# Performance work log

Measured on AMD Instinct MI355X. Metric: run time of the kernel, lower is better.

## Reference

```python
import jax, jax.numpy as jnp
import numpy as np

NUM_POINTS = 100000
BATCH = 4096
K = 10


def setup_inputs() -> dict:
    key = jax.random.key(0)
    k1, k2, k3, k4, k5 = jax.random.split(key, 5)
    rays_o = jax.random.normal(k1, (BATCH, 3), dtype=jnp.float32)
    rays_d = jax.random.normal(k2, (BATCH, 3), dtype=jnp.float32)
    xyz = jax.random.normal(k3, (NUM_POINTS, 3), dtype=jnp.float32) * 0.1
    features_dc = jax.random.normal(k4, (NUM_POINTS, 1, 3), dtype=jnp.float32)
    opacity = jax.random.normal(k5, (NUM_POINTS, 1), dtype=jnp.float32)
    return {"rays_o": rays_o, "rays_d": rays_d, "xyz": xyz,
            "features_dc": features_dc, "opacity": opacity}


def reference(rays_o, rays_d, xyz, features_dc, opacity):
    # colors = sigmoid(features[:,0,:]) ; features[:,0,:] == features_dc[:,0,:]
    colors = jax.nn.sigmoid(features_dc[:, 0, :])          # [N,3]
    op = jax.nn.sigmoid(opacity[:, 0])                      # [N]
    ray_centers = rays_o + rays_d * 3.0                     # [B,3]
    # Euclidean cdist via ||a||^2 + ||b||^2 - 2 a.b (matmul form, like torch.cdist p=2)
    sq = (jnp.sum(ray_centers * ray_centers, axis=1)[:, None]
          + jnp.sum(xyz * xyz, axis=1)[None, :]
          - 2.0 * ray_centers @ xyz.T)                      # [B,N]
    distances = jnp.sqrt(jnp.maximum(sq, 0.0))
    # top-K smallest distances per ray
    _, idx = jax.lax.top_k(-distances, K)                   # [B,K]
    d_sel = jnp.take_along_axis(distances, idx, axis=1)     # [B,K]
    w = jnp.exp(-d_sel * 0.1) * op[idx]                     # [B,K]
    w = w / (jnp.sum(w, axis=1, keepdims=True) + 1e-8)
    rgb = jnp.einsum('bk,bkc->bc', w, colors[idx])          # [B,3]
    return rgb
```

## Files before the change

### kernel.cpp

```cpp
#include <hip/hip_runtime.h>
#include <math.h>

#define NPTS    100000
#define NRAYS   4096
#define KTOP    10
#define KMER    12
#define CAP     128

#define GCELLS  4096
#define RCAP    256
#define DMARGIN 1e-3f
#define NB      64
#define PPB     1568

#define TPAIR   4
#define NPART   64
#define TRAYS   8
#define TGRP    16

typedef float v2f __attribute__((ext_vector_type(2)));
typedef unsigned int u32;
typedef unsigned short u16;

static_assert(TGRP * 2048 <= NPTS, "theta sample within real points");
static_assert(NB * PPB >= NPTS, "binning covers all points");

__device__ __forceinline__ float4 make_center(const float* __restrict__ ro,
                                              const float* __restrict__ rd,
                                              int ray, float w) {
    float ox = ro[3 * ray + 0], oy = ro[3 * ray + 1], oz = ro[3 * ray + 2];
    float dx = rd[3 * ray + 0], dy = rd[3 * ray + 1], dz = rd[3 * ray + 2];
    float cx, cy, cz;
    {
#pragma clang fp contract(off)
        cx = ox + dx * 3.0f;
        cy = oy + dy * 3.0f;
        cz = oz + dz * 3.0f;
    }
    return make_float4(cx, cy, cz, w);
}

__device__ __forceinline__ float sigm(float x) { return 1.0f / (1.0f + expf(-x)); }

__device__ __forceinline__ float rfl(float x) {
    return __int_as_float(__builtin_amdgcn_readfirstlane(__float_as_int(x)));
}

__device__ __forceinline__ v2f score2(v2f px, v2f py, v2f pz, v2f pw,
                                      v2f rx, v2f ry, v2f rz) {
    v2f t = __builtin_elementwise_fma(pz, rz, pw);
    t = __builtin_elementwise_fma(py, ry, t);
    return __builtin_elementwise_fma(px, rx, t);
}

__device__ __forceinline__ unsigned long long mkkey(float sc, int id, bool v) {
    unsigned u = __float_as_uint(sc);
    u = (u & 0x80000000u) ? ~u : (u | 0x80000000u);
    unsigned long long k = ((unsigned long long)u << 32) | (unsigned)(~id);
    return v ? k : 0ull;
}

__device__ __forceinline__ int cellcoord(float x) {
    int v = (int)floorf((x + 0.8f) * 10.0f);
    return v < 0 ? 0 : (v > 15 ? 15 : v);
}

__global__ __launch_bounds__(256, 2) void theta_kernel(const float* __restrict__ xyz,
                                                       const float* __restrict__ ro,
                                                       const float* __restrict__ rd,
                                                       float4* __restrict__ c4,
                                                       int* __restrict__ cnt) {
    __shared__ float4 rsh[TRAYS];
    __shared__ float  Msh[4][TRAYS][64];
    const int tid = threadIdx.x, wave = tid >> 6, lane = tid & 63;
    const int rbase = blockIdx.x * TRAYS;

    if (tid < TRAYS) rsh[tid] = make_center(ro, rd, rbase + tid, 0.0f);
    __syncthreads();

    float4 rr[TRAYS];
#pragma unroll
    for (int r = 0; r < TRAYS; ++r) rr[r] = rsh[r];

    v2f M[TRAYS];
#pragma unroll
    for (int r = 0; r < TRAYS; ++r) M[r] = (v2f){-INFINITY, -INFINITY};

    v2f pxA[TPAIR], pyA[TPAIR], pzA[TPAIR], pwA[TPAIR];
    v2f pxB[TPAIR], pyB[TPAIR], pzB[TPAIR], pwB[TPAIR];

    auto loadg = [&](v2f* PX, v2f* PY, v2f* PZ, v2f* PW, int g) {
        const int id0 = g * 2048 + wave * 512 + lane;
#pragma unroll
        for (int u = 0; u < TPAIR; ++u) {
            int ia = id0 + (2 * u) * 64, ib = id0 + (2 * u + 1) * 64;
            float xa = xyz[3 * ia + 0], ya = xyz[3 * ia + 1], za = xyz[3 * ia + 2];
            float xb = xyz[3 * ib + 0], yb = xyz[3 * ib + 1], zb = xyz[3 * ib + 2];
            PX[u] = (v2f){xa, xb}; PY[u] = (v2f){ya, yb}; PZ[u] = (v2f){za, zb};
            PW[u] = (v2f){-0.5f * fmaf(xa, xa, fmaf(ya, ya, za * za)),
                          -0.5f * fmaf(xb, xb, fmaf(yb, yb, zb * zb))};
        }
    };
    auto computeg = [&](const v2f* PX, const v2f* PY, const v2f* PZ, const v2f* PW) {
#pragma unroll
        for (int r = 0; r < TRAYS; ++r) {
            const v2f rx = (v2f){rr[r].x, rr[r].x};
            const v2f ry = (v2f){rr[r].y, rr[r].y};
            const v2f rz = (v2f){rr[r].z, rr[r].z};
            v2f m = M[r];
#pragma unroll
            for (int u = 0; u < TPAIR; ++u)
                m = __builtin_elementwise_max(m, score2(PX[u], PY[u], PZ[u], PW[u], rx, ry, rz));
            M[r] = m;
        }
    };

    loadg(pxA, pyA, pzA, pwA, 0);
#pragma unroll 1
    for (int g = 0; g < TGRP; g += 2) {
        loadg(pxB, pyB, pzB, pwB, g + 1);
        computeg(pxA, pyA, pzA, pwA);
        if (g + 2 < TGRP) loadg(pxA, pyA, pzA, pwA, g + 2);
        computeg(pxB, pyB, pzB, pwB);
    }

#pragma unroll
    for (int r = 0; r < TRAYS; ++r)
        Msh[wave][r][lane] = fmaxf(M[r].x, M[r].y);
    __syncthreads();

    if (tid < TRAYS) {
        float vs[KTOP];
#pragma unroll
        for (int j = 0; j < KTOP; ++j) vs[j] = -INFINITY;
#pragma unroll 1
        for (int p = 0; p < NPART; ++p) {
            float v = fmaxf(fmaxf(Msh[0][tid][p], Msh[1][tid][p]),
                            fmaxf(Msh[2][tid][p], Msh[3][tid][p]));
#pragma unroll
            for (int t = KTOP - 1; t >= 1; --t) {
                bool up = v > vs[t - 1], here = v > vs[t];
                vs[t] = up ? vs[t - 1] : (here ? v : vs[t]);
            }
            vs[0] = fmaxf(vs[0], v);
        }
        float4 c = rsh[tid];
        c.w = vs[KTOP - 1];
        c4[rbase + tid] = c;
        cnt[rbase + tid] = 0;
    }
}

__global__ __launch_bounds__(256) void hist_kernel(const float* __restrict__ xyz,
                                                   u32* __restrict__ mat,
                                                   u16* __restrict__ cid16) {
    __shared__ u32 h[GCELLS];
    const int b = blockIdx.x, tid = threadIdx.x;
    for (int c = tid; c < GCELLS; c += 256) h[c] = 0;
    __syncthreads();
    const int s = b * PPB, e = (s + PPB < NPTS) ? s + PPB : NPTS;
    for (int i = s + tid; i < e; i += 256) {
        float x = xyz[3 * i + 0], y = xyz[3 * i + 1], z = xyz[3 * i + 2];
        int cid = (cellcoord(x) << 8) | (cellcoord(y) << 4) | cellcoord(z);
        cid16[i] = (u16)cid;
        atomicAdd(&h[cid], 1u);
    }
    __syncthreads();
    u32* row = mat + (size_t)b * GCELLS;
    for (int c = tid; c < GCELLS; c += 256) row[c] = h[c];
}

__global__ __launch_bounds__(256) void colsum_kernel(const u32* __restrict__ mat,
                                                     u32* __restrict__ cellcnt) {
    const int c = blockIdx.x * 256 + threadIdx.x;
    u32 s = 0;
#pragma unroll 4
    for (int b = 0; b < NB; ++b) s += mat[(size_t)b * GCELLS + c];
    cellcnt[c] = s;
}

__global__ __launch_bounds__(256) void prefix_kernel(const u32* __restrict__ cellcnt,
                                                     u32* __restrict__ cellstart) {
    __shared__ u32 wsum[4];
    const int tid = threadIdx.x, wave = tid >> 6, lane = tid & 63;
    const int base = tid * 16;
    u32 loc[16]; u32 s = 0;
#pragma unroll
    for (int k = 0; k < 16; ++k) { loc[k] = cellcnt[base + k]; s += loc[k]; }
    u32 v = s;
#pragma unroll
    for (int off = 1; off < 64; off <<= 1) {
        u32 o = __shfl_up(v, off);
        if (lane >= off) v += o;
    }
    if (lane == 63) wsum[wave] = v;
    __syncthreads();
    u32 woff = 0;
    for (int w = 0; w < 4; ++w) if (w < wave) woff += wsum[w];
    u32 run = woff + v - s;
#pragma unroll
    for (int k = 0; k < 16; ++k) {
        cellstart[base + k] = run;
        run += loc[k];
    }
    if (tid == 255) cellstart[4096] = run;
}

__global__ __launch_bounds__(256) void offs_kernel(u32* __restrict__ mat,
                                                   const u32* __restrict__ cellstart) {
    const int c = blockIdx.x * 256 + threadIdx.x;
    u32 run = cellstart[c];
#pragma unroll 4
    for (int b = 0; b < NB; ++b) {
        size_t idx = (size_t)b * GCELLS + c;
        u32 v = mat[idx];
        mat[idx] = run;
        run += v;
    }
}

__global__ __launch_bounds__(256) void scatter_kernel(const float* __restrict__ xyz,
                                                      const u16* __restrict__ cid16,
                                                      const u32* __restrict__ mat,
                                                      float4* __restrict__ pts4,
                                                      int* __restrict__ pid) {
    __shared__ u32 cur[GCELLS];
    const int b = blockIdx.x, tid = threadIdx.x;
    const u32* row = mat + (size_t)b * GCELLS;
    for (int c = tid; c < GCELLS; c += 256) cur[c] = row[c];
    __syncthreads();
    const int s = b * PPB, e = (s + PPB < NPTS) ? s + PPB : NPTS;
    for (int i = s + tid; i < e; i += 256) {
        int cid = cid16[i];
        u32 dst = atomicAdd(&cur[cid], 1u);
        float x = xyz[3 * i + 0], y = xyz[3 * i + 1], z = xyz[3 * i + 2];
        pts4[dst] = make_float4(x, y, z, -0.5f * fmaf(x, x, fmaf(y, y, z * z)));
        pid[dst] = i;
    }
}

__global__ __launch_bounds__(256) void scan_kernel(const float4* __restrict__ pts4,
                                                   const int* __restrict__ pid,
                                                   const u32* __restrict__ cellstart,
                                                   const float4* __restrict__ c4,
                                                   int* __restrict__ cnt,
                                                   float2* __restrict__ cand) {
    __shared__ u32    runS[4][RCAP], runE[4][RCAP];
    __shared__ float2 lbuf[4][CAP];
    __shared__ float  axd2[4][3][16];
    __shared__ int    nrun[4], lcnt[4];
    const int tid = threadIdx.x, w = tid >> 6, lane = tid & 63;
    const int ray = blockIdx.x * 4 + w;

    float4 q = c4[ray];
    const float cx = rfl(q.x), cy = rfl(q.y), cz = rfl(q.z), th = rfl(q.w);
    const float limit = fmaf(cx, cx, fmaf(cy, cy, cz * cz)) - 2.0f * th + DMARGIN;

    if (lane == 0) { nrun[w] = 0; lcnt[w] = 0; }
    if (lane < 48) {
        const int ax = lane >> 4, i = lane & 15;
        const float cc = (ax == 0) ? cx : ((ax == 1) ? cy : cz);
        const float lo = (i == 0)  ? -3.0e38f : -0.8f + 0.1f * (float)i;
        const float hi = (i == 15) ?  3.0e38f : -0.8f + 0.1f * (float)(i + 1);
        const float d = fmaxf(fmaxf(lo - cc, cc - hi), 0.0f);
        axd2[w][ax][i] = d * d;
    }
    __syncthreads();

#pragma unroll 1
    for (int cc4 = 0; cc4 < 4; ++cc4) {
        const int col = lane + cc4 * 64;
        const float base2 = axd2[w][0][col >> 4] + axd2[w][1][col & 15];
        u32 mask = 0;
        if (base2 <= limit) {
#pragma unroll
            for (int iz = 0; iz < 16; ++iz)
                mask |= (base2 + axd2[w][2][iz] <= limit) ? (1u << iz) : 0u;
        }
        const int colbase = col << 4;
        while (mask) {
            int lo = __ffs(mask) - 1;
            u32 t = mask >> lo;
            int len = __ffs(~t) - 1;
            mask &= ~(((1u << len) - 1u) << lo);
            u32 s = cellstart[colbase + lo];
            u32 e = cellstart[colbase + lo + len];
            if (e > s) {
                int slot = atomicAdd(&nrun[w], 1);
                if (slot < RCAP) { runS[w][slot] = s; runE[w][slot] = e; }
            }
        }
    }
    __syncthreads();

    int NR = nrun[w];
    const bool fb = NR > RCAP;
    if (fb) NR = 1;
#pragma unroll 1
    for (int ri = 0; ri < NR; ++ri) {
        u32 s = fb ? 0u : runS[w][ri];
        u32 e = fb ? (u32)NPTS : runE[w][ri];
        for (u32 j = s + lane; j < e; j += 64) {
            float4 p = pts4[j];
            float sc = fmaf(p.x, cx, fmaf(p.y, cy, fmaf(p.z, cz, p.w)));
            if (sc >= th) {
                int slot = atomicAdd(&lcnt[w], 1);
                if (slot < CAP) lbuf[w][slot] = make_float2(sc, __int_as_float(pid[j]));
            }
        }
    }
    __syncthreads();

    int n = lcnt[w];
    int m = n < CAP ? n : CAP;
    for (int j = lane; j < m; j += 64) cand[(ray << 7) + j] = lbuf[w][j];
    if (lane == 0) cnt[ray] = n;
}

__global__ __launch_bounds__(256) void merge_kernel(const float* __restrict__ ro,
                                                    const float* __restrict__ rd,
                                                    const int* __restrict__ cnt,
                                                    const float2* __restrict__ cand,
                                                    const float* __restrict__ xyz,
                                                    const float* __restrict__ fdc,
                                                    const float* __restrict__ opac,
                                                    float* __restrict__ out) {
    const int wave = threadIdx.x >> 6, lane = threadIdx.x & 63;
    const int ray = blockIdx.x * 4 + wave;

    int n = cnt[ray];
    n = n < CAP ? n : CAP;

    const float2* cl = cand + (ray << 7);
    float2 e0 = cl[lane];
    float2 e1 = cl[64 + lane];
    int id0 = __float_as_int(e0.y), id1 = __float_as_int(e1.y);

    unsigned long long k0 = mkkey(e0.x, id0, lane < n);
    unsigned long long k1 = mkkey(e1.x, id1, lane + 64 < n);

    int sel = -1;
    unsigned long long kl = k0 > k1 ? k0 : k1;
#pragma unroll
    for (int j = 0; j < KMER; ++j) {
        unsigned long long m = kl;
#pragma unroll
        for (int off = 1; off < 64; off <<= 1) {
            unsigned long long o = __shfl_xor(m, off);
            m = m > o ? m : o;
        }
        bool win = (kl == m) && (m != 0ull);
        int wid = (k0 >= k1) ? id0 : id1;
        unsigned long long wmask = __ballot(win);
        int wl = __ffsll(wmask) - 1;
        int bid = __shfl(wid, wl & 63);
        if (m == 0ull) bid = -1;
        if (lane == j) sel = bid;
        if (win) {
            if (k0 >= k1) k0 = 0ull; else k1 = 0ull;
            kl = k0 > k1 ? k0 : k1;
        }
    }

    float ox = ro[3 * ray + 0], oy = ro[3 * ray + 1], oz = ro[3 * ray + 2];
    float dx = rd[3 * ray + 0], dy = rd[3 * ray + 1], dz = rd[3 * ray + 2];
    float cxf, cyf, czf;
    {
#pragma clang fp contract(off)
        cxf = ox + dx * 3.0f;
        cyf = oy + dy * 3.0f;
        czf = oz + dz * 3.0f;
    }
    double Cx = (double)cxf, Cy = (double)cyf, Cz = (double)czf;
    double cn = Cx * Cx + Cy * Cy + Cz * Cz;

    bool valid = (lane < KMER) && (sel >= 0);
    int pidv = valid ? sel : 0;
    double X = (double)xyz[3 * pidv + 0];
    double Y = (double)xyz[3 * pidv + 1];
    double Z = (double)xyz[3 * pidv + 2];
    double sq = valid ? (cn + (X * X + Y * Y + Z * Z) - 2.0 * (Cx * X + Cy * Y + Cz * Z))
                      : (double)INFINITY;
    int cid = valid ? sel : 0x7fffffff;

    int rank = 0;
#pragma unroll
    for (int k = 0; k < KMER; ++k) {
        double sk = __shfl(sq, k);
        int    ik = __shfl(cid, k);
        if ((sk < sq) || (sk == sq && ik < cid)) ++rank;
    }

    bool take = valid && (rank < KTOP);
    float w = 0.0f, rr = 0.0f, gg = 0.0f, bb = 0.0f;
    if (take) {
        float dd = sqrtf(fmaxf((float)sq, 0.0f));
        w  = expf(-0.1f * dd) * sigm(opac[pidv]);
        rr = w * sigm(fdc[3 * pidv + 0]);
        gg = w * sigm(fdc[3 * pidv + 1]);
        bb = w * sigm(fdc[3 * pidv + 2]);
    }
#pragma unroll
    for (int off = 1; off < 64; off <<= 1) {
        w  += __shfl_xor(w,  off);
        rr += __shfl_xor(rr, off);
        gg += __shfl_xor(gg, off);
        bb += __shfl_xor(bb, off);
    }
    if (lane == 0) {
        float inv = 1.0f / (w + 1e-8f);
        out[3 * ray + 0] = rr * inv;
        out[3 * ray + 1] = gg * inv;
        out[3 * ray + 2] = bb * inv;
    }
}

extern "C" void kernel_launch(void* const* d_in, const int* in_sizes, int n_in,
                              void* d_out, int out_size, void* d_ws, size_t ws_size,
                              hipStream_t stream) {
    const float* rays_o = (const float*)d_in[0];
    const float* rays_d = (const float*)d_in[1];
    const float* xyz    = (const float*)d_in[2];
    const float* fdc    = (const float*)d_in[3];
    const float* opac   = (const float*)d_in[4];
    float* out = (float*)d_out;

    char* p = (char*)d_ws;
    float4* c4       = (float4*)p;  p += (size_t)NRAYS  * 16;
    float4* pts4     = (float4*)p;  p += (size_t)(NPTS + 64) * 16;
    float2* cand     = (float2*)p;  p += (size_t)NRAYS * CAP * 8;
    u32*    mat      = (u32*)p;     p += (size_t)NB * GCELLS * 4;
    u32*    cellcnt  = (u32*)p;     p += (size_t)GCELLS * 4;
    u32*    cellstart= (u32*)p;     p += (size_t)4112 * 4;
    int*    cnt      = (int*)p;     p += (size_t)NRAYS * 4;
    int*    pid      = (int*)p;     p += (size_t)(NPTS + 64) * 4;
    u16*    cid16    = (u16*)p;     p += (size_t)(NPTS + 64) * 2;

    theta_kernel<<<NRAYS / TRAYS, 256, 0, stream>>>(xyz, rays_o, rays_d, c4, cnt);
    hist_kernel<<<NB, 256, 0, stream>>>(xyz, mat, cid16);
    colsum_kernel<<<GCELLS / 256, 256, 0, stream>>>(mat, cellcnt);
    prefix_kernel<<<1, 256, 0, stream>>>(cellcnt, cellstart);
    offs_kernel<<<GCELLS / 256, 256, 0, stream>>>(mat, cellstart);
    scatter_kernel<<<NB, 256, 0, stream>>>(xyz, cid16, mat, pts4, pid);
    scan_kernel<<<NRAYS / 4, 256, 0, stream>>>(pts4, pid, cellstart, c4, cnt, cand);
    merge_kernel<<<NRAYS / 4, 256, 0, stream>>>(rays_o, rays_d, cnt, cand, xyz, fdc, opac, out);
}
```

Before: 158.3 us.

## Fuse pipeline stages to cut kernel launches from eight to four

Folds the histogram pass into the theta kernel, running on the first NB blocks. Merges colsum, prefix and offset passes into a single one-block meta kernel, and fuses the scan and merge kernels so candidates stay in shared memory. This removes launch gaps and the global round trip for candidate buffers and counts. The risks are that the one-block meta kernel serialises the column sums and offset writes over 64x4096 entries, and that theta blocks now carry an extra 16KB of shared memory.

After: 220.1 us. +39.0%, slower.

```diff
diff --git a/kernel.cpp b/kernel.cpp
--- a/kernel.cpp
+++ b/kernel.cpp
@@ -65,13 +65,15 @@
     return v < 0 ? 0 : (v > 15 ? 15 : v);
 }
 
-__global__ __launch_bounds__(256, 2) void theta_kernel(const float* __restrict__ xyz,
-                                                       const float* __restrict__ ro,
-                                                       const float* __restrict__ rd,
-                                                       float4* __restrict__ c4,
-                                                       int* __restrict__ cnt) {
+__global__ __launch_bounds__(256, 2) void theta_hist_kernel(const float* __restrict__ xyz,
+                                                            const float* __restrict__ ro,
+                                                            const float* __restrict__ rd,
+                                                            float4* __restrict__ c4,
+                                                            u32* __restrict__ mat,
+                                                            u16* __restrict__ cid16) {
     __shared__ float4 rsh[TRAYS];
     __shared__ float  Msh[4][TRAYS][64];
+    __shared__ u32    h[GCELLS];
     const int tid = threadIdx.x, wave = tid >> 6, lane = tid & 63;
     const int rbase = blockIdx.x * TRAYS;
 
@@ -147,46 +149,43 @@
         float4 c = rsh[tid];
         c.w = vs[KTOP - 1];
         c4[rbase + tid] = c;
-        cnt[rbase + tid] = 0;
-    }
-}
-
-__global__ __launch_bounds__(256) void hist_kernel(const float* __restrict__ xyz,
-                                                   u32* __restrict__ mat,
-                                                   u16* __restrict__ cid16) {
-    __shared__ u32 h[GCELLS];
-    const int b = blockIdx.x, tid = threadIdx.x;
-    for (int c = tid; c < GCELLS; c += 256) h[c] = 0;
-    __syncthreads();
-    const int s = b * PPB, e = (s + PPB < NPTS) ? s + PPB : NPTS;
-    for (int i = s + tid; i < e; i += 256) {
-        float x = xyz[3 * i + 0], y = xyz[3 * i + 1], z = xyz[3 * i + 2];
-        int cid = (cellcoord(x) << 8) | (cellcoord(y) << 4) | cellcoord(z);
-        cid16[i] = (u16)cid;
-        atomicAdd(&h[cid], 1u);
-    }
-    __syncthreads();
-    u32* row = mat + (size_t)b * GCELLS;
-    for (int c = tid; c < GCELLS; c += 256) row[c] = h[c];
-}
-
-__global__ __launch_bounds__(256) void colsum_kernel(const u32* __restrict__ mat,
-                                                     u32* __restrict__ cellcnt) {
-    const int c = blockIdx.x * 256 + threadIdx.x;
-    u32 s = 0;
-#pragma unroll 4
-    for (int b = 0; b < NB; ++b) s += mat[(size_t)b * GCELLS + c];
-    cellcnt[c] = s;
-}
-
-__global__ __launch_bounds__(256) void prefix_kernel(const u32* __restrict__ cellcnt,
-                                                     u32* __restrict__ cellstart) {
+    }
+
+    if (blockIdx.x < NB) {
+        const int b = blockIdx.x;
+        for (int c = tid; c < GCELLS; c += 256) h[c] = 0;
+        __syncthreads();
+        const int s = b * PPB, e = (s + PPB < NPTS) ? s + PPB : NPTS;
+        for (int i = s + tid; i < e; i += 256) {
+            float x = xyz[3 * i + 0], y = xyz[3 * i + 1], z = xyz[3 * i + 2];
+            int cid = (cellcoord(x) << 8) | (cellcoord(y) << 4) | cellcoord(z);
+            cid16[i] = (u16)cid;
+            atomicAdd(&h[cid], 1u);
+        }
+        __syncthreads();
+        u32* row = mat + (size_t)b * GCELLS;
+        for (int c = tid; c < GCELLS; c += 256) row[c] = h[c];
+    }
+}
+
+__global__ __launch_bounds__(256) void meta_kernel(u32* __restrict__ mat,
+                                                   u32* __restrict__ cellstart) {
+    __shared__ u32 cc[GCELLS];
     __shared__ u32 wsum[4];
     const int tid = threadIdx.x, wave = tid >> 6, lane = tid & 63;
+
+    for (int c = tid; c < GCELLS; c += 256) {
+        u32 s = 0;
+#pragma unroll 4
+        for (int b = 0; b < NB; ++b) s += mat[(size_t)b * GCELLS + c];
+        cc[c] = s;
+    }
+    __syncthreads();
+
     const int base = tid * 16;
     u32 loc[16]; u32 s = 0;
 #pragma unroll
-    for (int k = 0; k < 16; ++k) { loc[k] = cellcnt[base + k]; s += loc[k]; }
+    for (int k = 0; k < 16; ++k) { loc[k] = cc[base + k]; s += loc[k]; }
     u32 v = s;
 #pragma unroll
     for (int off = 1; off < 64; off <<= 1) {
@@ -201,21 +200,23 @@
 #pragma unroll
     for (int k = 0; k < 16; ++k) {
         cellstart[base + k] = run;
+        cc[base + k] = run;
         run += loc[k];
     }
     if (tid == 255) cellstart[4096] = run;
-}
-
-__global__ __launch_bounds__(256) void offs_kernel(u32* __restrict__ mat,
-                                                   const u32* __restrict__ cellstart) {
-    const int c = blockIdx.x * 256 + threadIdx.x;
-    u32 run = cellstart[c];
+    __syncthreads();
+
+#pragma unroll 1
+    for (int j = 0; j < 16; ++j) {
+        const int c = tid + 256 * j;
+        u32 r2 = cc[c];
 #pragma unroll 4
-    for (int b = 0; b < NB; ++b) {
-        size_t idx = (size_t)b * GCELLS + c;
-        u32 v = mat[idx];
-        mat[idx] = run;
-        run += v;
+        for (int b = 0; b < NB; ++b) {
+            size_t idx = (size_t)b * GCELLS + c;
+            u32 t = mat[idx];
+            mat[idx] = r2;
+            r2 += t;
+        }
     }
 }
 
@@ -239,43 +240,47 @@
     }
 }
 
-__global__ __launch_bounds__(256) void scan_kernel(const float4* __restrict__ pts4,
-                                                   const int* __restrict__ pid,
-                                                   const u32* __restrict__ cellstart,
-                                                   const float4* __restrict__ c4,
-                                                   int* __restrict__ cnt,
-                                                   float2* __restrict__ cand) {
+__global__ __launch_bounds__(256) void scanmerge_kernel(const float4* __restrict__ pts4,
+                                                        const int* __restrict__ pid,
+                                                        const u32* __restrict__ cellstart,
+                                                        const float4* __restrict__ c4,
+                                                        const float* __restrict__ ro,
+                                                        const float* __restrict__ rd,
+                                                        const float* __restrict__ xyz,
+                                                        const float* __restrict__ fdc,
+                                                        const float* __restrict__ opac,
+                                                        float* __restrict__ out) {
     __shared__ u32    runS[4][RCAP], runE[4][RCAP];
     __shared__ float2 lbuf[4][CAP];
     __shared__ float  axd2[4][3][16];
     __shared__ int    nrun[4], lcnt[4];
-    const int tid = threadIdx.x, w = tid >> 6, lane = tid & 63;
-    const int ray = blockIdx.x * 4 + w;
+    const int tid = threadIdx.x, wv = tid >> 6, lane = tid & 63;
+    const int ray = blockIdx.x * 4 + wv;
 
     float4 q = c4[ray];
     const float cx = rfl(q.x), cy = rfl(q.y), cz = rfl(q.z), th = rfl(q.w);
     const float limit = fmaf(cx, cx, fmaf(cy, cy, cz * cz)) - 2.0f * th + DMARGIN;
 
-    if (lane == 0) { nrun[w] = 0; lcnt[w] = 0; }
+    if (lane == 0) { nrun[wv] = 0; lcnt[wv] = 0; }
     if (lane < 48) {
         const int ax = lane >> 4, i = lane & 15;
         const float cc = (ax == 0) ? cx : ((ax == 1) ? cy : cz);
         const float lo = (i == 0)  ? -3.0e38f : -0.8f + 0.1f * (float)i;
         const float hi = (i == 15) ?  3.0e38f : -0.8f + 0.1f * (float)(i + 1);
         const float d = fmaxf(fmaxf(lo - cc, cc - hi), 0.0f);
-        axd2[w][ax][i] = d * d;
+        axd2[wv][ax][i] = d * d;
     }
     __syncthreads();
 
 #pragma unroll 1
     for (int cc4 = 0; cc4 < 4; ++cc4) {
         const int col = lane + cc4 * 64;
-        const float base2 = axd2[w][0][col >> 4] + axd2[w][1][col & 15];
+        const float base2 = axd2[wv][0][col >> 4] + axd2[wv][1][col & 15];
         u32 mask = 0;
         if (base2 <= limit) {
 #pragma unroll
             for (int iz = 0; iz < 16; ++iz)
-                mask |= (base2 + axd2[w][2][iz] <= limit) ? (1u << iz) : 0u;
+                mask |= (base2 + axd2[wv][2][iz] <= limit) ? (1u << iz) : 0u;
         }
         const int colbase = col << 4;
         while (mask) {
@@ -286,54 +291,36 @@
             u32 s = cellstart[colbase + lo];
             u32 e = cellstart[colbase + lo + len];
             if (e > s) {
-                int slot = atomicAdd(&nrun[w], 1);
-                if (slot < RCAP) { runS[w][slot] = s; runE[w][slot] = e; }
+                int slot = atomicAdd(&nrun[wv], 1);
+                if (slot < RCAP) { runS[wv][slot] = s; runE[wv][slot] = e; }
             }
         }
     }
     __syncthreads();
 
-    int NR = nrun[w];
+    int NR = nrun[wv];
     const bool fb = NR > RCAP;
     if (fb) NR = 1;
 #pragma unroll 1
     for (int ri = 0; ri < NR; ++ri) {
-        u32 s = fb ? 0u : runS[w][ri];
-        u32 e = fb ? (u32)NPTS : runE[w][ri];
+        u32 s = fb ? 0u : runS[wv][ri];
+        u32 e = fb ? (u32)NPTS : runE[wv][ri];
         for (u32 j = s + lane; j < e; j += 64) {
             float4 p = pts4[j];
             float sc = fmaf(p.x, cx, fmaf(p.y, cy, fmaf(p.z, cz, p.w)));
             if (sc >= th) {
-                int slot = atomicAdd(&lcnt[w], 1);
-                if (slot < CAP) lbuf[w][slot] = make_float2(sc, __int_as_float(pid[j]));
+                int slot = atomicAdd(&lcnt[wv], 1);
+                if (slot < CAP) lbuf[wv][slot] = make_float2(sc, __int_as_float(pid[j]));
             }
         }
     }
     __syncthreads();
 
-    int n = lcnt[w];
-    int m = n < CAP ? n : CAP;
-    for (int j = lane; j < m; j += 64) cand[(ray << 7) + j] = lbuf[w][j];
-    if (lane == 0) cnt[ray] = n;
-}
-
-__global__ __launch_bounds__(256) void merge_kernel(const float* __restrict__ ro,
-                                                    const float* __restrict__ rd,
-                                                    const int* __restrict__ cnt,
-                                                    const float2* __restrict__ cand,
-                                                    const float* __restrict__ xyz,
-                                                    const float* __restrict__ fdc,
-                                                    const float* __restrict__ opac,
-                                                    float* __restrict__ out) {
-    const int wave = threadIdx.x >> 6, lane = threadIdx.x & 63;
-    const int ray = blockIdx.x * 4 + wave;
-
-    int n = cnt[ray];
+    int n = lcnt[wv];
     n = n < CAP ? n : CAP;
 
-    const float2* cl = cand + (ray << 7);
-    float2 e0 = cl[lane];
-    float2 e1 = cl[64 + lane];
+    float2 e0 = lbuf[wv][lane];
+    float2 e1 = lbuf[wv][64 + lane];
     int id0 = __float_as_int(e0.y), id1 = __float_as_int(e1.y);
 
     unsigned long long k0 = mkkey(e0.x, id0, lane < n);
@@ -428,20 +415,14 @@
     char* p = (char*)d_ws;
     float4* c4       = (float4*)p;  p += (size_t)NRAYS  * 16;
     float4* pts4     = (float4*)p;  p += (size_t)(NPTS + 64) * 16;
-    float2* cand     = (float2*)p;  p += (size_t)NRAYS * CAP * 8;
     u32*    mat      = (u32*)p;     p += (size_t)NB * GCELLS * 4;
-    u32*    cellcnt  = (u32*)p;     p += (size_t)GCELLS * 4;
     u32*    cellstart= (u32*)p;     p += (size_t)4112 * 4;
-    int*    cnt      = (int*)p;     p += (size_t)NRAYS * 4;
     int*    pid      = (int*)p;     p += (size_t)(NPTS + 64) * 4;
     u16*    cid16    = (u16*)p;     p += (size_t)(NPTS + 64) * 2;
 
-    theta_kernel<<<NRAYS / TRAYS, 256, 0, stream>>>(xyz, rays_o, rays_d, c4, cnt);
-    hist_kernel<<<NB, 256, 0, stream>>>(xyz, mat, cid16);
-    colsum_kernel<<<GCELLS / 256, 256, 0, stream>>>(mat, cellcnt);
-    prefix_kernel<<<1, 256, 0, stream>>>(cellcnt, cellstart);
-    offs_kernel<<<GCELLS / 256, 256, 0, stream>>>(mat, cellstart);
+    theta_hist_kernel<<<NRAYS / TRAYS, 256, 0, stream>>>(xyz, rays_o, rays_d, c4, mat, cid16);
+    meta_kernel<<<1, 256, 0, stream>>>(mat, cellstart);
     scatter_kernel<<<NB, 256, 0, stream>>>(xyz, cid16, mat, pts4, pid);
-    scan_kernel<<<NRAYS / 4, 256, 0, stream>>>(pts4, pid, cellstart, c4, cnt, cand);
-    merge_kernel<<<NRAYS / 4, 256, 0, stream>>>(rays_o, rays_d, cnt, cand, xyz, fdc, opac, out);
-}
+    scanmerge_kernel<<<NRAYS / 4, 256, 0, stream>>>(pts4, pid, cellstart, c4,
+                                                    rays_o, rays_d, xyz, fdc, opac, out);
+}
```
